# Kernel optimization log

Measured on AMD Instinct MI355X. Metric: run time of the kernel, lower is better.

The kernel has to match this reference:

```python
import jax, jax.numpy as jnp
import numpy as np

N_GRID = 16       # n
CELL_SIDE = 2.0
LATENT = 16       # latent_dim (pooling_dim for type_='social')
HIDDEN = 128
OUT_DIM = 128
CONSTANT = 0.0
NUM_TRACKS = 1024


def setup_inputs() -> dict:
    key = jax.random.key(0)
    ks = jax.random.split(key, 6)
    T = NUM_TRACKS
    hidden_state = jax.random.normal(ks[0], (T, HIDDEN), jnp.float32)
    # positions spread over a ~20m scene; obs2 is obs1 plus a small step (velocity)
    obs1 = jax.random.uniform(ks[1], (T, 2), jnp.float32) * 20.0
    obs2 = obs1 + jax.random.normal(ks[2], (T, 2), jnp.float32) * 0.5
    W_enc = jax.random.normal(ks[3], (HIDDEN, LATENT), jnp.float32) / np.sqrt(HIDDEN)
    b_enc = jnp.zeros((LATENT,), jnp.float32)
    in_dim = N_GRID * N_GRID * LATENT  # 4096
    W_emb = jax.random.normal(ks[4], (in_dim, OUT_DIM), jnp.float32) / np.sqrt(in_dim)
    b_emb = jnp.zeros((OUT_DIM,), jnp.float32)
    return dict(hidden_state=hidden_state, obs1=obs1, obs2=obs2,
                W_enc=W_enc, b_enc=b_enc, W_emb=W_emb, b_emb=b_emb)


def _social_grid(hidden_state, obs2, W_enc, b_enc):
    T = obs2.shape[0]
    # NaN rows -> 0 (mask = isnan(obs).any(dim=1))
    obs = jnp.where(jnp.isnan(obs2).any(axis=1, keepdims=True), 0.0, obs2)
    # static off-diagonal neighbor indices: row i lists all j != i  [T, T-1]
    cols = np.broadcast_to(np.arange(T), (T, T))
    nbr = cols[~np.eye(T, dtype=bool)].reshape(T, T - 1)
    rel = obs[nbr] - obs[:, None, :]                 # [T, T-1, 2] obs[j]-obs[i]
    vals = hidden_state[nbr] @ W_enc + b_enc         # [T, T-1, LATENT]
    # grid cell coordinates (pool_size=1, front=False)
    oij = rel / CELL_SIDE + N_GRID / 2.0             # [T, T-1, 2]
    in_range = jnp.sum((oij < 0) | (oij >= N_GRID), axis=2) == 0  # [T, T-1]
    oij_i = jnp.where(in_range[..., None], oij, 0.0).astype(jnp.int32)
    vals = jnp.where(in_range[..., None], vals, CONSTANT)
    oi = oij_i[..., 0] * N_GRID + oij_i[..., 1]      # flat cell index [T, T-1]
    occ = jnp.full((T, N_GRID * N_GRID, LATENT), CONSTANT, vals.dtype)
    occ = occ.at[jnp.arange(T)[:, None], oi].set(vals)
    # [T, LATENT, n, n]; blur_size=1 and lp_pool with kernel=pool_size=1 are identity
    return jnp.transpose(occ, (0, 2, 1)).reshape(T, LATENT, N_GRID, N_GRID)


def reference(hidden_state, obs1, obs2, W_enc, b_enc, W_emb, b_emb):
    grid = _social_grid(hidden_state, obs2, W_enc, b_enc)
    T = grid.shape[0]
    flat = grid.reshape(T, -1)                       # [T, n*n*LATENT]
    return jax.nn.relu(flat @ W_emb + b_emb)         # [T, OUT_DIM]
```

## Files before the change

### kernel.cpp

```cpp
#include <hip/hip_runtime.h>
#include <hip/hip_bf16.h>
#include <math.h>

#define T_TRACKS 1024
#define HIDDEN 128
#define LATENT 16
#define NGRID 16
#define NCELLS 256
#define KDIM 4096
#define OUTD 128

typedef unsigned short ushort_t;
typedef __attribute__((ext_vector_type(8))) short frag_ab;
typedef __attribute__((ext_vector_type(4))) float f32x4;

static __device__ inline ushort_t f2bf(float x) {
    __hip_bfloat16 h = __float2bfloat16(x);
    return *reinterpret_cast<ushort_t*>(&h);
}

#define WS_VALS 0
#define WS_WT   32768
#define WS_OCC  1081344
#define WS_PART 9469952
#define WS_NEED (9469952 + 8388608)

__global__ __launch_bounds__(256) void prep_kernel(const float* __restrict__ hidden,
                                                   const float* __restrict__ W_enc,
                                                   const float* __restrict__ b_enc,
                                                   const float* __restrict__ W_emb,
                                                   ushort_t* __restrict__ vals_bf16,
                                                   ushort_t* __restrict__ W_t) {
    const int b = blockIdx.x;
    const int tid = threadIdx.x;
    if (b < 64) {
        int idx = b * 256 + tid;
        int j = idx >> 4, l = idx & 15;
        const float* h = hidden + j * HIDDEN;
        float acc = b_enc[l];
#pragma unroll 8
        for (int k = 0; k < HIDDEN; k++) acc += h[k] * W_enc[k * LATENT + l];
        vals_bf16[idx] = f2bf(acc);
    } else {
        int idx = (b - 64) * 256 + tid;
        int kc = idx >> 7;
        int o = idx & 127;
        ushort_t tmp[8];
#pragma unroll
        for (int u = 0; u < 8; u++) tmp[u] = f2bf(W_emb[(kc * 8 + u) * OUTD + o]);
        *reinterpret_cast<uint4*>(W_t + o * KDIM + kc * 8) = *reinterpret_cast<uint4*>(tmp);
    }
}

__global__ __launch_bounds__(256) void occ_kernel(const float* __restrict__ obs2,
                                                  const ushort_t* __restrict__ vals_bf16,
                                                  ushort_t* __restrict__ occ) {
    const int i = blockIdx.x;
    const int tid = threadIdx.x;
    __shared__ int owner[NCELLS];
    __shared__ ushort_t socc[LATENT * NCELLS];
    owner[tid] = -1;

    float oix = obs2[i * 2 + 0];
    float oiy = obs2[i * 2 + 1];
    if (isnan(oix) || isnan(oiy)) { oix = 0.0f; oiy = 0.0f; }
    __syncthreads();

    for (int j = tid; j < T_TRACKS; j += 256) {
        if (j == i) continue;
        float ox = obs2[j * 2 + 0];
        float oy = obs2[j * 2 + 1];
        if (isnan(ox) || isnan(oy)) { ox = 0.0f; oy = 0.0f; }
        float gx = (ox - oix) * 0.5f + 8.0f;
        float gy = (oy - oiy) * 0.5f + 8.0f;
        bool inr = (gx >= 0.0f) && (gx < 16.0f) && (gy >= 0.0f) && (gy < 16.0f);
        int c = inr ? ((int)gx * NGRID + (int)gy) : 0;
        atomicMax(&owner[c], j);
    }
    __syncthreads();

    {
        const int c = tid;
        int j = owner[c];
        bool valid = (j >= 0);
        if (c == 0 && valid) {
            float ox = obs2[j * 2 + 0];
            float oy = obs2[j * 2 + 1];
            if (isnan(ox) || isnan(oy)) { ox = 0.0f; oy = 0.0f; }
            float gx = (ox - oix) * 0.5f + 8.0f;
            float gy = (oy - oiy) * 0.5f + 8.0f;
            valid = (gx >= 0.0f) && (gx < 16.0f) && (gy >= 0.0f) && (gy < 16.0f);
        }
        int jj = (j >= 0) ? j : 0;
        ushort_t vv[16];
        *reinterpret_cast<uint4*>(vv)     = *reinterpret_cast<const uint4*>(vals_bf16 + jj * LATENT);
        *reinterpret_cast<uint4*>(vv + 8) = *reinterpret_cast<const uint4*>(vals_bf16 + jj * LATENT + 8);
#pragma unroll
        for (int l = 0; l < LATENT; l++) {
            socc[l * NCELLS + c] = valid ? vv[l] : (ushort_t)0;
        }
    }
    __syncthreads();

    uint4* dst = reinterpret_cast<uint4*>(occ + i * KDIM);
    const uint4* src = reinterpret_cast<const uint4*>(socc);
    dst[tid]       = src[tid];
    dst[tid + 256] = src[tid + 256];
}

#define BK 128
#define LDSTR 136
__global__ __launch_bounds__(256) void gemm_kernel(const ushort_t* __restrict__ occ,
                                                   const ushort_t* __restrict__ W_t,
                                                   float* __restrict__ partial) {
    const int tid = threadIdx.x;
    const int kt = blockIdx.x & 15;
    const int mt = blockIdx.x >> 4;
    const int wave = tid >> 6;
    const int lane = tid & 63;
    const int lrow = lane & 15;
    const int quad = lane >> 4;

    __shared__ ushort_t As[64 * LDSTR];
    __shared__ ushort_t Bs[128 * LDSTR];

    f32x4 acc[8];
#pragma unroll
    for (int nt = 0; nt < 8; nt++) acc[nt] = (f32x4){0.f, 0.f, 0.f, 0.f};

    for (int chunk = 0; chunk < 2; chunk++) {
        const int k0 = kt * 256 + chunk * BK;
        for (int g = tid; g < 1024; g += 256) {
            int r = g >> 4, cs = g & 15;
            uint4 v = *reinterpret_cast<const uint4*>(occ + (mt * 64 + r) * KDIM + k0 + cs * 8);
            *reinterpret_cast<uint4*>(As + r * LDSTR + cs * 8) = v;
        }
        for (int g = tid; g < 2048; g += 256) {
            int n = g >> 4, cs = g & 15;
            uint4 v = *reinterpret_cast<const uint4*>(W_t + n * KDIM + k0 + cs * 8);
            *reinterpret_cast<uint4*>(Bs + n * LDSTR + cs * 8) = v;
        }
        __syncthreads();
#pragma unroll
        for (int ks = 0; ks < 4; ks++) {
            const int koff = ks * 32 + quad * 8;
            frag_ab a = *reinterpret_cast<const frag_ab*>(&As[(wave * 16 + lrow) * LDSTR + koff]);
#pragma unroll
            for (int nt = 0; nt < 8; nt++) {
                frag_ab bfr = *reinterpret_cast<const frag_ab*>(&Bs[(nt * 16 + lrow) * LDSTR + koff]);
                acc[nt] = __builtin_amdgcn_mfma_f32_16x16x32_bf16(a, bfr, acc[nt], 0, 0, 0);
            }
        }
        __syncthreads();
    }
    float* pt = partial + (size_t)kt * (T_TRACKS * OUTD) + (mt * 64) * OUTD;
#pragma unroll
    for (int nt = 0; nt < 8; nt++) {
        int n = nt * 16 + lrow;
#pragma unroll
        for (int reg = 0; reg < 4; reg++) {
            int m = wave * 16 + quad * 4 + reg;
            pt[m * OUTD + n] = acc[nt][reg];
        }
    }
}

__global__ __launch_bounds__(256) void reduce_kernel(const float* __restrict__ partial,
                                                     const float* __restrict__ b_emb,
                                                     float* __restrict__ out) {
    int idx = blockIdx.x * 256 + threadIdx.x;
    const float4* p4 = reinterpret_cast<const float4*>(partial);
    float4 s = p4[idx];
#pragma unroll
    for (int kt = 1; kt < 16; kt++) {
        float4 v = p4[kt * 32768 + idx];
        s.x += v.x; s.y += v.y; s.z += v.z; s.w += v.w;
    }
    float4 bv = reinterpret_cast<const float4*>(b_emb)[idx & 31];
    float4 r;
    r.x = fmaxf(s.x + bv.x, 0.0f);
    r.y = fmaxf(s.y + bv.y, 0.0f);
    r.z = fmaxf(s.z + bv.z, 0.0f);
    r.w = fmaxf(s.w + bv.w, 0.0f);
    reinterpret_cast<float4*>(out)[idx] = r;
}

__global__ __launch_bounds__(256) void vals_kernel_f32(const float* __restrict__ hidden,
                                                       const float* __restrict__ W_enc,
                                                       const float* __restrict__ b_enc,
                                                       float* __restrict__ vals) {
    int idx = blockIdx.x * 256 + threadIdx.x;
    int j = idx >> 4, l = idx & 15;
    const float* h = hidden + j * HIDDEN;
    float acc = b_enc[l];
#pragma unroll 8
    for (int k = 0; k < HIDDEN; k++) acc += h[k] * W_enc[k * LATENT + l];
    vals[idx] = acc;
}

__global__ __launch_bounds__(256) void pool_kernel_f32(const float* __restrict__ obs2,
                                                       const float* __restrict__ vals,
                                                       const float* __restrict__ W_emb,
                                                       const float* __restrict__ b_emb,
                                                       float* __restrict__ out) {
    const int i = blockIdx.x;
    const int tid = threadIdx.x;
    __shared__ int owner[NCELLS];
    __shared__ float occ[NCELLS * LATENT];
    __shared__ float partial[OUTD];
    owner[tid] = -1;
    float oix = obs2[i * 2 + 0];
    float oiy = obs2[i * 2 + 1];
    if (isnan(oix) || isnan(oiy)) { oix = 0.0f; oiy = 0.0f; }
    __syncthreads();
    for (int j = tid; j < T_TRACKS; j += 256) {
        if (j == i) continue;
        float ox = obs2[j * 2 + 0], oy = obs2[j * 2 + 1];
        if (isnan(ox) || isnan(oy)) { ox = 0.0f; oy = 0.0f; }
        float gx = (ox - oix) * 0.5f + 8.0f;
        float gy = (oy - oiy) * 0.5f + 8.0f;
        bool inr = (gx >= 0.0f) && (gx < 16.0f) && (gy >= 0.0f) && (gy < 16.0f);
        int c = inr ? ((int)gx * NGRID + (int)gy) : 0;
        atomicMax(&owner[c], j);
    }
    __syncthreads();
    {
        int j = owner[tid];
        bool valid = false;
        if (j >= 0) {
            float ox = obs2[j * 2 + 0], oy = obs2[j * 2 + 1];
            if (isnan(ox) || isnan(oy)) { ox = 0.0f; oy = 0.0f; }
            float gx = (ox - oix) * 0.5f + 8.0f;
            float gy = (oy - oiy) * 0.5f + 8.0f;
            valid = (gx >= 0.0f) && (gx < 16.0f) && (gy >= 0.0f) && (gy < 16.0f);
        }
        const float* vj = vals + (j >= 0 ? j : 0) * LATENT;
#pragma unroll
        for (int l = 0; l < LATENT; l++) occ[tid * LATENT + l] = valid ? vj[l] : 0.0f;
    }
    __syncthreads();
    const int o = tid & (OUTD - 1);
    const int half = tid >> 7;
    const int cbase = half * 128;
    float acc = 0.0f;
    for (int c = cbase; c < cbase + 128; c++) {
#pragma unroll
        for (int l = 0; l < LATENT; l++)
            acc += occ[c * LATENT + l] * W_emb[(l * NCELLS + c) * OUTD + o];
    }
    if (half == 0) partial[o] = acc;
    __syncthreads();
    if (half == 1) out[i * OUTD + o] = fmaxf(acc + partial[o] + b_emb[o], 0.0f);
}

extern "C" void kernel_launch(void* const* d_in, const int* in_sizes, int n_in,
                              void* d_out, int out_size, void* d_ws, size_t ws_size,
                              hipStream_t stream) {
    const float* hidden = (const float*)d_in[0];
    const float* obs2   = (const float*)d_in[2];
    const float* W_enc  = (const float*)d_in[3];
    const float* b_enc  = (const float*)d_in[4];
    const float* W_emb  = (const float*)d_in[5];
    const float* b_emb  = (const float*)d_in[6];
    float* out = (float*)d_out;

    if (ws_size < (size_t)WS_NEED) {
        float* vals = (float*)d_ws;
        vals_kernel_f32<<<(T_TRACKS * LATENT) / 256, 256, 0, stream>>>(hidden, W_enc, b_enc, vals);
        pool_kernel_f32<<<T_TRACKS, 256, 0, stream>>>(obs2, vals, W_emb, b_emb, out);
        return;
    }

    char* ws = (char*)d_ws;
    ushort_t* vals_bf16 = (ushort_t*)(ws + WS_VALS);
    ushort_t* W_t       = (ushort_t*)(ws + WS_WT);
    ushort_t* occ       = (ushort_t*)(ws + WS_OCC);
    float*    partial   = (float*)(ws + WS_PART);

    prep_kernel<<<320, 256, 0, stream>>>(hidden, W_enc, b_enc, W_emb, vals_bf16, W_t);
    occ_kernel<<<T_TRACKS, 256, 0, stream>>>(obs2, vals_bf16, occ);
    gemm_kernel<<<256, 256, 0, stream>>>(occ, W_t, partial);
    reduce_kernel<<<128, 256, 0, stream>>>(partial, b_emb, out);
}
```

Baseline: 89.98 us.

## Fuse occupancy, GEMM and reduction into one flag-synchronized persistent kernel

Merges the occ, gemm and reduce kernels into a single launch. The first 1024 blocks build occupancy rows and signal per-64-row-tile counters, and 512 GEMM blocks spin on those counters before computing. The last GEMM block to finish a row tile then does the split-K reduction with bias and ReLU. The GEMM now reads A and B fragments straight from global memory instead of staging them in LDS, and the split-K factor goes from 16 to 32. This removes two launch gaps and lets the GEMM overlap the occupancy build. The cost is spin-wait deadlock risk if the GEMM blocks get scheduled before the producer blocks, plus twice the partial-sum traffic.

Result: slower. 338.4 us (+276.1%).

```diff
diff --git a/kernel.cpp b/kernel.cpp
--- a/kernel.cpp
+++ b/kernel.cpp
@@ -23,14 +23,16 @@
 #define WS_WT   32768
 #define WS_OCC  1081344
 #define WS_PART 9469952
-#define WS_NEED (9469952 + 8388608)
+#define WS_FLAG 26247168
+#define WS_NEED (26247168 + 256)
 
 __global__ __launch_bounds__(256) void prep_kernel(const float* __restrict__ hidden,
                                                    const float* __restrict__ W_enc,
                                                    const float* __restrict__ b_enc,
                                                    const float* __restrict__ W_emb,
                                                    ushort_t* __restrict__ vals_bf16,
-                                                   ushort_t* __restrict__ W_t) {
+                                                   ushort_t* __restrict__ W_t,
+                                                   int* __restrict__ flags) {
     const int b = blockIdx.x;
     const int tid = threadIdx.x;
     if (b < 64) {
@@ -49,110 +51,116 @@
 #pragma unroll
         for (int u = 0; u < 8; u++) tmp[u] = f2bf(W_emb[(kc * 8 + u) * OUTD + o]);
         *reinterpret_cast<uint4*>(W_t + o * KDIM + kc * 8) = *reinterpret_cast<uint4*>(tmp);
-    }
-}
-
-__global__ __launch_bounds__(256) void occ_kernel(const float* __restrict__ obs2,
-                                                  const ushort_t* __restrict__ vals_bf16,
-                                                  ushort_t* __restrict__ occ) {
-    const int i = blockIdx.x;
+        if (b == 319 && tid < 32) flags[tid] = 0;
+    }
+}
+
+__global__ __launch_bounds__(256, 4) void mega_kernel(const float* __restrict__ obs2,
+                                                      const ushort_t* __restrict__ vals_bf16,
+                                                      const ushort_t* __restrict__ W_t,
+                                                      ushort_t* __restrict__ occ,
+                                                      float* __restrict__ partial,
+                                                      int* __restrict__ flags,
+                                                      const float* __restrict__ b_emb,
+                                                      float* __restrict__ out) {
+    const int bid = blockIdx.x;
     const int tid = threadIdx.x;
+
     __shared__ int owner[NCELLS];
     __shared__ ushort_t socc[LATENT * NCELLS];
-    owner[tid] = -1;
-
-    float oix = obs2[i * 2 + 0];
-    float oiy = obs2[i * 2 + 1];
-    if (isnan(oix) || isnan(oiy)) { oix = 0.0f; oiy = 0.0f; }
-    __syncthreads();
-
-    for (int j = tid; j < T_TRACKS; j += 256) {
-        if (j == i) continue;
-        float ox = obs2[j * 2 + 0];
-        float oy = obs2[j * 2 + 1];
-        if (isnan(ox) || isnan(oy)) { ox = 0.0f; oy = 0.0f; }
-        float gx = (ox - oix) * 0.5f + 8.0f;
-        float gy = (oy - oiy) * 0.5f + 8.0f;
-        bool inr = (gx >= 0.0f) && (gx < 16.0f) && (gy >= 0.0f) && (gy < 16.0f);
-        int c = inr ? ((int)gx * NGRID + (int)gy) : 0;
-        atomicMax(&owner[c], j);
-    }
-    __syncthreads();
-
-    {
-        const int c = tid;
-        int j = owner[c];
-        bool valid = (j >= 0);
-        if (c == 0 && valid) {
+    __shared__ int bcast;
+
+    if (bid < T_TRACKS) {
+        const int i = bid;
+        owner[tid] = -1;
+        float oix = obs2[i * 2 + 0];
+        float oiy = obs2[i * 2 + 1];
+        if (isnan(oix) || isnan(oiy)) { oix = 0.0f; oiy = 0.0f; }
+        __syncthreads();
+
+        for (int j = tid; j < T_TRACKS; j += 256) {
+            if (j == i) continue;
             float ox = obs2[j * 2 + 0];
             float oy = obs2[j * 2 + 1];
             if (isnan(ox) || isnan(oy)) { ox = 0.0f; oy = 0.0f; }
             float gx = (ox - oix) * 0.5f + 8.0f;
             float gy = (oy - oiy) * 0.5f + 8.0f;
-            valid = (gx >= 0.0f) && (gx < 16.0f) && (gy >= 0.0f) && (gy < 16.0f);
-        }
-        int jj = (j >= 0) ? j : 0;
-        ushort_t vv[16];
-        *reinterpret_cast<uint4*>(vv)     = *reinterpret_cast<const uint4*>(vals_bf16 + jj * LATENT);
-        *reinterpret_cast<uint4*>(vv + 8) = *reinterpret_cast<const uint4*>(vals_bf16 + jj * LATENT + 8);
-#pragma unroll
-        for (int l = 0; l < LATENT; l++) {
-            socc[l * NCELLS + c] = valid ? vv[l] : (ushort_t)0;
-        }
-    }
-    __syncthreads();
-
-    uint4* dst = reinterpret_cast<uint4*>(occ + i * KDIM);
-    const uint4* src = reinterpret_cast<const uint4*>(socc);
-    dst[tid]       = src[tid];
-    dst[tid + 256] = src[tid + 256];
-}
-
-#define BK 128
-#define LDSTR 136
-__global__ __launch_bounds__(256) void gemm_kernel(const ushort_t* __restrict__ occ,
-                                                   const ushort_t* __restrict__ W_t,
-                                                   float* __restrict__ partial) {
-    const int tid = threadIdx.x;
-    const int kt = blockIdx.x & 15;
-    const int mt = blockIdx.x >> 4;
+            bool inr = (gx >= 0.0f) && (gx < 16.0f) && (gy >= 0.0f) && (gy < 16.0f);
+            int c = inr ? ((int)gx * NGRID + (int)gy) : 0;
+            atomicMax(&owner[c], j);
+        }
+        __syncthreads();
+
+        {
+            const int c = tid;
+            int j = owner[c];
+            bool valid = (j >= 0);
+            if (c == 0 && valid) {
+                float ox = obs2[j * 2 + 0];
+                float oy = obs2[j * 2 + 1];
+                if (isnan(ox) || isnan(oy)) { ox = 0.0f; oy = 0.0f; }
+                float gx = (ox - oix) * 0.5f + 8.0f;
+                float gy = (oy - oiy) * 0.5f + 8.0f;
+                valid = (gx >= 0.0f) && (gx < 16.0f) && (gy >= 0.0f) && (gy < 16.0f);
+            }
+            int jj = (j >= 0) ? j : 0;
+            ushort_t vv[16];
+            *reinterpret_cast<uint4*>(vv)     = *reinterpret_cast<const uint4*>(vals_bf16 + jj * LATENT);
+            *reinterpret_cast<uint4*>(vv + 8) = *reinterpret_cast<const uint4*>(vals_bf16 + jj * LATENT + 8);
+#pragma unroll
+            for (int l = 0; l < LATENT; l++) {
+                socc[l * NCELLS + c] = valid ? vv[l] : (ushort_t)0;
+            }
+        }
+        __syncthreads();
+
+        uint4* dst = reinterpret_cast<uint4*>(occ + (size_t)i * KDIM);
+        const uint4* src = reinterpret_cast<const uint4*>(socc);
+        dst[tid]       = src[tid];
+        dst[tid + 256] = src[tid + 256];
+
+        __syncthreads();
+        __threadfence();
+        if (tid == 0) {
+            __hip_atomic_fetch_add(&flags[i >> 6], 1, __ATOMIC_RELEASE, __HIP_MEMORY_SCOPE_AGENT);
+        }
+        return;
+    }
+
+    const int g = bid - T_TRACKS;
+    const int kt = g & 31;
+    const int mt = g >> 5;
     const int wave = tid >> 6;
     const int lane = tid & 63;
     const int lrow = lane & 15;
     const int quad = lane >> 4;
 
-    __shared__ ushort_t As[64 * LDSTR];
-    __shared__ ushort_t Bs[128 * LDSTR];
-
+    if (tid == 0) {
+        while (__hip_atomic_load(&flags[mt], __ATOMIC_ACQUIRE, __HIP_MEMORY_SCOPE_AGENT) < 64) {
+            __builtin_amdgcn_s_sleep(8);
+        }
+        bcast = 1;
+    }
+    __syncthreads();
+    __threadfence();
+
+    const int k0 = kt * 128;
     f32x4 acc[8];
 #pragma unroll
     for (int nt = 0; nt < 8; nt++) acc[nt] = (f32x4){0.f, 0.f, 0.f, 0.f};
 
-    for (int chunk = 0; chunk < 2; chunk++) {
-        const int k0 = kt * 256 + chunk * BK;
-        for (int g = tid; g < 1024; g += 256) {
-            int r = g >> 4, cs = g & 15;
-            uint4 v = *reinterpret_cast<const uint4*>(occ + (mt * 64 + r) * KDIM + k0 + cs * 8);
-            *reinterpret_cast<uint4*>(As + r * LDSTR + cs * 8) = v;
-        }
-        for (int g = tid; g < 2048; g += 256) {
-            int n = g >> 4, cs = g & 15;
-            uint4 v = *reinterpret_cast<const uint4*>(W_t + n * KDIM + k0 + cs * 8);
-            *reinterpret_cast<uint4*>(Bs + n * LDSTR + cs * 8) = v;
-        }
-        __syncthreads();
-#pragma unroll
-        for (int ks = 0; ks < 4; ks++) {
-            const int koff = ks * 32 + quad * 8;
-            frag_ab a = *reinterpret_cast<const frag_ab*>(&As[(wave * 16 + lrow) * LDSTR + koff]);
-#pragma unroll
-            for (int nt = 0; nt < 8; nt++) {
-                frag_ab bfr = *reinterpret_cast<const frag_ab*>(&Bs[(nt * 16 + lrow) * LDSTR + koff]);
-                acc[nt] = __builtin_amdgcn_mfma_f32_16x16x32_bf16(a, bfr, acc[nt], 0, 0, 0);
-            }
-        }
-        __syncthreads();
-    }
+    const ushort_t* arow = occ + (size_t)(mt * 64 + wave * 16 + lrow) * KDIM + k0 + quad * 8;
+    const ushort_t* brow = W_t + (size_t)lrow * KDIM + k0 + quad * 8;
+#pragma unroll
+    for (int ks = 0; ks < 4; ks++) {
+        frag_ab a = *reinterpret_cast<const frag_ab*>(arow + ks * 32);
+#pragma unroll
+        for (int nt = 0; nt < 8; nt++) {
+            frag_ab bf = *reinterpret_cast<const frag_ab*>(brow + (size_t)nt * 16 * KDIM + ks * 32);
+            acc[nt] = __builtin_amdgcn_mfma_f32_16x16x32_bf16(a, bf, acc[nt], 0, 0, 0);
+        }
+    }
+
     float* pt = partial + (size_t)kt * (T_TRACKS * OUTD) + (mt * 64) * OUTD;
 #pragma unroll
     for (int nt = 0; nt < 8; nt++) {
@@ -163,26 +171,35 @@
             pt[m * OUTD + n] = acc[nt][reg];
         }
     }
-}
-
-__global__ __launch_bounds__(256) void reduce_kernel(const float* __restrict__ partial,
-                                                     const float* __restrict__ b_emb,
-                                                     float* __restrict__ out) {
-    int idx = blockIdx.x * 256 + threadIdx.x;
+
+    __syncthreads();
+    __threadfence();
+    if (tid == 0) {
+        int old = __hip_atomic_fetch_add(&flags[16 + mt], 1, __ATOMIC_ACQ_REL, __HIP_MEMORY_SCOPE_AGENT);
+        bcast = (old == 31);
+    }
+    __syncthreads();
+    if (!bcast) return;
+    __threadfence();
+
     const float4* p4 = reinterpret_cast<const float4*>(partial);
-    float4 s = p4[idx];
-#pragma unroll
-    for (int kt = 1; kt < 16; kt++) {
-        float4 v = p4[kt * 32768 + idx];
-        s.x += v.x; s.y += v.y; s.z += v.z; s.w += v.w;
-    }
-    float4 bv = reinterpret_cast<const float4*>(b_emb)[idx & 31];
-    float4 r;
-    r.x = fmaxf(s.x + bv.x, 0.0f);
-    r.y = fmaxf(s.y + bv.y, 0.0f);
-    r.z = fmaxf(s.z + bv.z, 0.0f);
-    r.w = fmaxf(s.w + bv.w, 0.0f);
-    reinterpret_cast<float4*>(out)[idx] = r;
+    const float4* b4 = reinterpret_cast<const float4*>(b_emb);
+    float4* o4 = reinterpret_cast<float4*>(out);
+    for (int idx = tid; idx < 2048; idx += 256) {
+        float4 s = p4[(size_t)mt * 2048 + idx];
+#pragma unroll
+        for (int k = 1; k < 32; k++) {
+            float4 v = p4[(size_t)k * 32768 + mt * 2048 + idx];
+            s.x += v.x; s.y += v.y; s.z += v.z; s.w += v.w;
+        }
+        float4 bv = b4[idx & 31];
+        float4 r;
+        r.x = fmaxf(s.x + bv.x, 0.0f);
+        r.y = fmaxf(s.y + bv.y, 0.0f);
+        r.z = fmaxf(s.z + bv.z, 0.0f);
+        r.w = fmaxf(s.w + bv.w, 0.0f);
+        o4[mt * 2048 + idx] = r;
+    }
 }
 
 __global__ __launch_bounds__(256) void vals_kernel_f32(const float* __restrict__ hidden,
@@ -276,9 +293,9 @@
     ushort_t* W_t       = (ushort_t*)(ws + WS_WT);
     ushort_t* occ       = (ushort_t*)(ws + WS_OCC);
     float*    partial   = (float*)(ws + WS_PART);
-
-    prep_kernel<<<320, 256, 0, stream>>>(hidden, W_enc, b_enc, W_emb, vals_bf16, W_t);
-    occ_kernel<<<T_TRACKS, 256, 0, stream>>>(obs2, vals_bf16, occ);
-    gemm_kernel<<<256, 256, 0, stream>>>(occ, W_t, partial);
-    reduce_kernel<<<128, 256, 0, stream>>>(partial, b_emb, out);
-}
+    int*      flags     = (int*)(ws + WS_FLAG);
+
+    prep_kernel<<<320, 256, 0, stream>>>(hidden, W_enc, b_enc, W_emb, vals_bf16, W_t, flags);
+    mega_kernel<<<T_TRACKS + 512, 256, 0, stream>>>(obs2, vals_bf16, W_t, occ, partial,
+                                                    flags, b_emb, out);
+}
```
